# Performance work log

Hardware: AMD Instinct MI355X
Metric: run time of the kernel (lower is better)

## Reference

```python
import jax, jax.numpy as jnp
import numpy as np

B, L, C, W, NH, FS = 8, 8, 64, 32, 128, 5
PAD = FS // 2
LN_EPS = 1e-5


def _conv(x, w, b, pad):
    y = jax.lax.conv_general_dilated(x, w, (1, 1), [(pad, pad), (pad, pad)],
                                     dimension_numbers=('NCHW', 'OIHW', 'NCHW'))
    return y + b[None, :, None, None]


def _stem(x, w1, b1, lnw, lnb, w2, b2):
    # conv(fs) -> LayerNorm over [C,W,W] -> ReLU -> conv(1x1)
    y = _conv(x, w1, b1, PAD)
    mu = jnp.mean(y, axis=(1, 2, 3), keepdims=True)
    var = jnp.var(y, axis=(1, 2, 3), keepdims=True)
    y = (y - mu) * jax.lax.rsqrt(var + LN_EPS) * lnw[None] + lnb[None]
    return _conv(jax.nn.relu(y), w2, b2, 0)


def setup_inputs() -> dict:
    key = jax.random.key(0)
    ks = jax.random.split(key, 8)
    f = lambda k, shp: jax.random.normal(k, shp, jnp.float32) * 0.02
    return {
        'in_query': jax.random.normal(ks[0], (B, C, W, W), jnp.float32),
        'in_keys': jax.random.normal(ks[1], (B, L, C, W, W), jnp.float32),
        'in_values': jax.random.normal(ks[2], (B, L, C, W, W), jnp.float32),
        's_w1': f(ks[3], (C, C, FS, FS)), 's_b1': jnp.zeros((C,), jnp.float32),
        's_lnw': jnp.ones((C, W, W), jnp.float32), 's_lnb': jnp.zeros((C, W, W), jnp.float32),
        's_w2': f(ks[4], (NH, C, 1, 1)), 's_b2': jnp.zeros((NH,), jnp.float32),
        'c_w1': f(ks[5], (C, C, FS, FS)), 'c_b1': jnp.zeros((C,), jnp.float32),
        'c_lnw': jnp.ones((C, W, W), jnp.float32), 'c_lnb': jnp.zeros((C, W, W), jnp.float32),
        'c_w2': f(ks[6], (NH, C, 1, 1)), 'c_b2': jnp.zeros((NH,), jnp.float32),
    }


def reference(in_query, in_keys, in_values,
              s_w1, s_b1, s_lnw, s_lnb, s_w2, s_b2,
              c_w1, c_b1, c_lnw, c_lnb, c_w2, c_b2):
    b, c, w, h = in_query.shape
    l = in_keys.shape[1]
    # ---- spatial attention: tokens = pixels, features = channels ----
    qf = in_query.reshape(b, c, w * h).transpose(0, 2, 1)            # [B, WH, C]
    kf = in_keys.transpose(0, 1, 3, 4, 2).reshape(b, l * w * h, c)   # [B, LWH, C]
    vf = in_values.transpose(0, 1, 3, 4, 2).reshape(b, l * w * h, c)
    a_sp = jax.nn.softmax(jnp.einsum('bnc,bmc->bnm', qf, kf), axis=-1)  # [B, WH, LWH]
    sp = jnp.einsum('bnm,bmc->bnc', a_sp, vf).reshape(b, w, h, c).transpose(0, 3, 1, 2)
    # ---- channel attention: tokens = channels, features = pixels ----
    qc = in_query.reshape(b, c, w * h)                               # [B, C, WH]
    kc = in_keys.reshape(b, l * c, h * w)                            # [B, LC, WH]
    vc = in_values.reshape(b, l * c, h * w)
    a_ch = jax.nn.softmax(jnp.einsum('bcn,bmn->bcm', qc, kc), axis=-1)  # [B, C, LC]
    ch = jnp.einsum('bcm,bmn->bcn', a_ch, vc).reshape(b, c, w, h)
    # ---- conv-LN-ReLU-conv stems on residual-added branches ----
    s_attn = _stem(sp + in_query, s_w1, s_b1, s_lnw, s_lnb, s_w2, s_b2)
    c_attn = _stem(ch + in_query, c_w1, c_b1, c_lnw, c_lnb, c_w2, c_b2)
    return (s_attn, c_attn)
```

## Files before the change

### kernel.cpp

```cpp
#include <hip/hip_runtime.h>


#define LOG2E 1.44269504088896340736f

typedef __attribute__((ext_vector_type(8))) short short8;
typedef __attribute__((ext_vector_type(4))) float f4;

#define MFMA16(a, b, c) __builtin_amdgcn_mfma_f32_16x16x32_bf16(a, b, c, 0, 0, 0)

#define GLOAD_LDS16(gp, lp) __builtin_amdgcn_global_load_lds( \
    (const __attribute__((address_space(1))) void*)(gp), \
    (__attribute__((address_space(3))) void*)(lp), 16, 0, 0)

__device__ __forceinline__ unsigned short f2bf(float f) {
  union { float f; unsigned u; } v; v.f = f;
  unsigned r = v.u + 0x7FFFu + ((v.u >> 16) & 1u);
  return (unsigned short)(r >> 16);
}
__device__ __forceinline__ unsigned short f2bf_rz(float f) {
  union { float f; unsigned u; } v; v.f = f;
  return (unsigned short)(v.u >> 16);
}
__device__ __forceinline__ float bf2f(unsigned short h) {
  union { unsigned u; float f; } v; v.u = ((unsigned)h) << 16;
  return v.f;
}
__device__ __forceinline__ float exp2fast(float x) {
#if __has_builtin(__builtin_amdgcn_exp2f)
  return __builtin_amdgcn_exp2f(x);
#else
  return exp2f(x);
#endif
}

#define O_STATS 0ul
#define O_W1T   256ul
#define O_W2B   409856ul
#define O_LNW   442624ul
#define O_LNB   704768ul
#define O_QT    966912ul
#define O_KSP   2015488ul
#define O_VT    10404096ul
#define O_NUM   18792704ul
#define O_DEN   35569920ul
#define O_SP    36094208ul
#define O_PCH   40288512ul
#define O_XS    40812800ul
#define O_XC    41861376ul
#define O_YT    42909952ul

__global__ __launch_bounds__(256) void k1_prep(
    const float* __restrict__ q, const float* __restrict__ keys,
    const float* __restrict__ values,
    const float* __restrict__ sw1, const float* __restrict__ slnw,
    const float* __restrict__ slnb, const float* __restrict__ sw2,
    const float* __restrict__ cw1, const float* __restrict__ clnw,
    const float* __restrict__ clnb, const float* __restrict__ cw2,
    char* __restrict__ ws)
{
  __shared__ float T[64][65];
  const int job = blockIdx.x, t = threadIdx.x;

  if (job < 2240) {
    int kind, mat = 0, sel = 0;
    if (job < 1024)      { kind = 0; mat = job >> 4; }
    else if (job < 2048) { kind = 1; mat = (job - 1024) >> 4; }
    else if (job < 2176) { kind = 2; mat = (job - 2048) >> 4; }
    else                 { kind = 3; sel = (job - 2176) >> 4; }
    const int pt = job & 15, p0 = pt * 64;
    const float* src =
        kind == 0 ? keys : kind == 1 ? values : kind == 2 ? q
        : (sel == 0 ? slnw : sel == 1 ? slnb : sel == 2 ? clnw : clnb);
    src += (size_t)mat * 65536;

    const int r0 = t >> 4, c4 = (t & 15) * 4;
    if (kind == 1) {
      unsigned short* VTp = (unsigned short*)(ws + O_VT);
      const int b = mat >> 3, l = mat & 7;
#pragma unroll
      for (int pass = 0; pass < 4; ++pass) {
        const int r = pass * 16 + r0;
        float4 v = *(const float4*)(src + (size_t)r * 1024 + p0 + c4);
        ushort4 o;
        o.x = f2bf(v.x); o.y = f2bf(v.y); o.z = f2bf(v.z); o.w = f2bf(v.w);
        *(ushort4*)(VTp + ((size_t)b * 64 + r) * 8192 + l * 1024 + p0 + c4) = o;
      }
      return;
    }
#pragma unroll
    for (int pass = 0; pass < 4; ++pass) {
      const int r = pass * 16 + r0;
      float4 v = *(const float4*)(src + (size_t)r * 1024 + p0 + c4);
      T[r][c4] = v.x; T[r][c4 + 1] = v.y; T[r][c4 + 2] = v.z; T[r][c4 + 3] = v.w;
    }
    __syncthreads();
#pragma unroll
    for (int pass = 0; pass < 2; ++pass) {
      const int p = pass * 32 + (t >> 3), cs = (t & 7) * 8;
      short8 o;
      if (kind == 0) {
#pragma unroll
        for (int j = 0; j < 8; ++j) o[j] = (short)f2bf(T[cs + j][p] * LOG2E);
        const int b = mat >> 3, l = mat & 7;
        *(short8*)((unsigned short*)(ws + O_KSP) +
                   ((size_t)b * 8192 + l * 1024 + p0 + p) * 64 + cs) = o;
      } else if (kind == 2) {
#pragma unroll
        for (int j = 0; j < 8; ++j) o[j] = (short)f2bf(T[cs + j][p]);
        *(short8*)((unsigned short*)(ws + O_QT) +
                   ((size_t)mat * 1024 + p0 + p) * 64 + cs) = o;
      } else {
#pragma unroll
        for (int j = 0; j < 8; ++j) o[j] = (short)f2bf(T[cs + j][p]);
        unsigned long off = (sel & 1) ? O_LNB : O_LNW;
        *(short8*)((unsigned short*)(ws + off) +
                   ((size_t)(sel >> 1) * 1024 + p0 + p) * 64 + cs) = o;
      }
    }
    return;
  }

  {
    unsigned i = (job - 2240) * 256u + t;
    if (i < 204800u) {
      unsigned ci = i & 63u, co = (i >> 6) & 63u, tt = i >> 12;
      unsigned off = tt % 25u, st = tt / 25u;
      const float* w = st ? cw1 : sw1;
      ((unsigned short*)(ws + O_W1T))[i] = f2bf(w[(co * 64u + ci) * 25u + off]);
      return;
    }
    i -= 204800u;
    if (i < 16384u) {
      unsigned c = i & 63u, nh = (i >> 6) & 127u, st = i >> 13;
      const float* w = st ? cw2 : sw2;
      ((unsigned short*)(ws + O_W2B))[i] = f2bf(w[nh * 64u + c]);
    }
  }
}

__global__ __launch_bounds__(256) void k2_spat_chanS(
    const float* __restrict__ q, const float* __restrict__ keys,
    char* __restrict__ ws)
{
  __shared__ __align__(16) unsigned char SM[65536];

  if (blockIdx.x < 512) {
    unsigned short (*Kt)[4096] = (unsigned short(*)[4096])(SM);
    unsigned short (*Vt)[4096] = (unsigned short(*)[4096])(SM + 16384);
    unsigned short (*Pl)[4096] = (unsigned short(*)[4096])(SM + 32768);

    const unsigned short* QT = (const unsigned short*)(ws + O_QT);
    const unsigned short* KSP = (const unsigned short*)(ws + O_KSP);
    const unsigned short* VTg = (const unsigned short*)(ws + O_VT);
    unsigned short* NUM = (unsigned short*)(ws + O_NUM);
    float* DEN = (float*)(ws + O_DEN);

    const int b = blockIdx.x >> 6;
    const int qt = (blockIdx.x >> 4) & 3;
    const int s = blockIdx.x & 15;
    const int t = threadIdx.x;
    const int w = t >> 6, lane = t & 63;
    const int low4 = lane & 15, quad = lane >> 4;

    const unsigned short* KSPb = KSP + (size_t)b * 8192 * 64;
    const unsigned short* VTb = VTg + (size_t)b * 64 * 8192;
    const int qbase = qt * 256 + w * 64;
    const int kvbase = s * 512;

    int cn[2], cks[2], cqd[2], cl4[2];
#pragma unroll
    for (int pass = 0; pass < 2; ++pass) {
      const int c = pass * 256 + t;
      cn[pass] = c >> 7; cks[pass] = (c >> 6) & 1;
      cqd[pass] = (c >> 4) & 3; cl4[pass] = c & 15;
    }

    short8 qa[4][2];
#pragma unroll
    for (int mi = 0; mi < 4; ++mi)
#pragma unroll
      for (int ks = 0; ks < 2; ++ks)
        qa[mi][ks] = *(const short8*)(QT +
            ((size_t)(b * 1024 + qbase + mi * 16 + low4)) * 64 + ks * 32 + quad * 8);

    short8 vones;
#pragma unroll
    for (int j = 0; j < 8; ++j) vones[j] = (short)0x3F80;

    f4 accO[4][4], accD[4];
#pragma unroll
    for (int m = 0; m < 4; ++m) {
      accD[m] = (f4){0.f, 0.f, 0.f, 0.f};
#pragma unroll
      for (int n = 0; n < 4; ++n) accO[m][n] = (f4){0.f, 0.f, 0.f, 0.f};
    }

#pragma unroll
    for (int pass = 0; pass < 2; ++pass) {
      GLOAD_LDS16(KSPb + ((size_t)(kvbase + cn[pass] * 16 + cl4[pass])) * 64 +
                      cks[pass] * 32 + cqd[pass] * 8,
                  &Kt[0][(pass * 256 + w * 64) * 8]);
      GLOAD_LDS16(VTb + ((size_t)(cn[pass] * 16 + cl4[pass])) * 8192 + kvbase +
                      cks[pass] * 32 + cqd[pass] * 8,
                  &Vt[0][(pass * 256 + w * 64) * 8]);
    }

    const int pswz = ((low4 >> 2) & 3) << 1;
    for (int it = 0; it < 8; ++it) {
      const int d = it & 1;
      __syncthreads();
      if (it < 7) {
        const int kv1 = kvbase + (it + 1) * 64;
#pragma unroll
        for (int pass = 0; pass < 2; ++pass) {
          GLOAD_LDS16(KSPb + ((size_t)(kv1 + cn[pass] * 16 + cl4[pass])) * 64 +
                          cks[pass] * 32 + cqd[pass] * 8,
                      &Kt[d ^ 1][(pass * 256 + w * 64) * 8]);
          GLOAD_LDS16(VTb + ((size_t)(cn[pass] * 16 + cl4[pass])) * 8192 + kv1 +
                          cks[pass] * 32 + cqd[pass] * 8,
                      &Vt[d ^ 1][(pass * 256 + w * 64) * 8]);
        }
      }
#pragma unroll
      for (int n = 0; n < 4; ++n) {
        f4 sS[4];
#pragma unroll
        for (int mi = 0; mi < 4; ++mi) sS[mi] = (f4){0.f, 0.f, 0.f, 0.f};
#pragma unroll
        for (int ks = 0; ks < 2; ++ks) {
          short8 kb = *(const short8*)&Kt[d][((n * 2 + ks) * 64 + lane) * 8];
#pragma unroll
          for (int mi = 0; mi < 4; ++mi) sS[mi] = MFMA16(qa[mi][ks], kb, sS[mi]);
        }
        const int cpr = (((n * 2 + (low4 >> 3)) ^ (quad << 1)) << 3) + (low4 & 7);
#pragma unroll
        for (int mi = 0; mi < 4; ++mi) {
          unsigned short* pw = &Pl[w][(mi * 16 + quad * 4) * 64 + cpr];
#pragma unroll
          for (int r = 0; r < 4; ++r)
            pw[r * 64] = f2bf_rz(exp2fast(sS[mi][r]));
        }
      }
#pragma unroll
      for (int ks = 0; ks < 2; ++ks) {
        short8 vb[4];
#pragma unroll
        for (int n2 = 0; n2 < 4; ++n2)
          vb[n2] = *(const short8*)&Vt[d][((n2 * 2 + ks) * 64 + lane) * 8];
        const int cr = (((ks * 4 + quad) ^ pswz) << 3);
#pragma unroll
        for (int m = 0; m < 4; ++m) {
          short8 pa = *(const short8*)&Pl[w][(m * 16 + low4) * 64 + cr];
          accD[m] = MFMA16(pa, vones, accD[m]);
#pragma unroll
          for (int n2 = 0; n2 < 4; ++n2) accO[m][n2] = MFMA16(pa, vb[n2], accO[m][n2]);
        }
      }
    }

#pragma unroll
    for (int m = 0; m < 4; ++m)
#pragma unroll
      for (int r = 0; r < 4; ++r) {
        const int row = qbase + m * 16 + quad * 4 + r;
        const size_t base = ((size_t)(b * 1024 + row) * 16 + s);
#pragma unroll
        for (int n2 = 0; n2 < 4; ++n2)
          NUM[base * 64 + n2 * 16 + low4] = f2bf(accO[m][n2][r]);
        if (low4 == 0) DEN[base] = accD[m][r];
      }
    return;
  }

  {
    float* Sp = (float*)(ws + O_SP);
    const int bid = blockIdx.x - 512;
    const int b = bid >> 4, colT = (bid >> 2) & 3, kt = bid & 3;
    const int t = threadIdx.x, w = t >> 6, lane = t & 63;
    const int low4 = lane & 15, quad = lane >> 4;
    const int dl = lane >> 1, dh = lane & 1;
    const int k00 = kt * 256;

    f4 acc[4][2];
#pragma unroll
    for (int m = 0; m < 4; ++m)
#pragma unroll
      for (int n = 0; n < 2; ++n) acc[m][n] = (f4){0.f, 0.f, 0.f, 0.f};

    auto stageAll = [&](int bo, int k0) {
#pragma unroll
      for (int gi = 0; gi < 4; ++gi) {
        const int g = w + gi * 4;
        const int n = g >> 1, sub = g & 1;
        const int l = sub * 32 + dl;
        const float* gp = keys + (size_t)(b * 512 + colT * 128 + n * 16 + (l & 15)) * 1024
                          + k0 + (l >> 4) * 8 + dh * 4;
        GLOAD_LDS16(gp, SM + bo + (size_t)(n * 128 + sub * 64) * 16);
      }
#pragma unroll
      for (int gi = 0; gi < 2; ++gi) {
        const int g = w + gi * 4;
        const int m = g >> 1, sub = g & 1;
        const int l = sub * 32 + dl;
        const float* gp = q + (size_t)(b * 64 + m * 16 + (l & 15)) * 1024
                          + k0 + (l >> 4) * 8 + dh * 4;
        GLOAD_LDS16(gp, SM + bo + 16384 + (size_t)(m * 128 + sub * 64) * 16);
      }
    };

    stageAll(0, k00);
    for (int it = 0; it < 8; ++it) {
      const int bo = (it & 1) * 24576;
      const char* cb = (const char*)SM + bo;
      __syncthreads();
      if (it < 7) stageAll(bo ^ 24576, k00 + (it + 1) * 32);

      short8 ah[4], al[4];
#pragma unroll
      for (int m = 0; m < 4; ++m) {
        const float* fp = (const float*)(cb + 16384 + (size_t)(m * 128 + lane * 2) * 16);
        float4 u0 = ((const float4*)fp)[0];
        float4 u1 = ((const float4*)fp)[1];
        float vv[8] = {u0.x, u0.y, u0.z, u0.w, u1.x, u1.y, u1.z, u1.w};
#pragma unroll
        for (int j = 0; j < 8; ++j) {
          float sv = vv[j] * LOG2E;
          unsigned short hi = f2bf(sv);
          ah[m][j] = (short)hi;
          al[m][j] = (short)f2bf(sv - bf2f(hi));
        }
      }
#pragma unroll
      for (int n2 = 0; n2 < 2; ++n2) {
        const int n = w * 2 + n2;
        const float* fp = (const float*)(cb + (size_t)(n * 128 + lane * 2) * 16);
        float4 u0 = ((const float4*)fp)[0];
        float4 u1 = ((const float4*)fp)[1];
        float vv[8] = {u0.x, u0.y, u0.z, u0.w, u1.x, u1.y, u1.z, u1.w};
        short8 bh, bl;
#pragma unroll
        for (int j = 0; j < 8; ++j) {
          unsigned short hi = f2bf(vv[j]);
          bh[j] = (short)hi;
          bl[j] = (short)f2bf(vv[j] - bf2f(hi));
        }
#pragma unroll
        for (int m = 0; m < 4; ++m) {
          acc[m][n2] = MFMA16(ah[m], bh, acc[m][n2]);
          acc[m][n2] = MFMA16(al[m], bh, acc[m][n2]);
          acc[m][n2] = MFMA16(ah[m], bl, acc[m][n2]);
        }
      }
    }

#pragma unroll
    for (int m = 0; m < 4; ++m)
#pragma unroll
      for (int n2 = 0; n2 < 2; ++n2)
#pragma unroll
        for (int r = 0; r < 4; ++r) {
          const int row = m * 16 + quad * 4 + r;
          const int col = colT * 128 + (w * 2 + n2) * 16 + low4;
          Sp[(((size_t)kt * 8 + b) * 64 + row) * 512 + col] = acc[m][n2][r];
        }
  }
}

__global__ __launch_bounds__(256) void k3_fin_soft(char* __restrict__ ws)
{
  if (blockIdx.x < 512) {
    const unsigned short* NUM = (const unsigned short*)(ws + O_NUM);
    const float* DEN = (const float*)(ws + O_DEN);
    const unsigned short* QT = (const unsigned short*)(ws + O_QT);
    unsigned short* Xs = (unsigned short*)(ws + O_XS);

    const unsigned i = blockIdx.x * 256u + threadIdx.x;
    const int c0 = (i & 15) * 4;
    const unsigned row = i >> 4;

    float dtot = 0.f;
#pragma unroll
    for (int sq = 0; sq < 4; ++sq) {
      float4 dv = *(const float4*)(DEN + (size_t)row * 16 + sq * 4);
      dtot += dv.x + dv.y + dv.z + dv.w;
    }
    float n4[4] = {0.f, 0.f, 0.f, 0.f};
#pragma unroll
    for (int s = 0; s < 16; ++s) {
      ushort4 pv = *(const ushort4*)(NUM + ((size_t)row * 16 + s) * 64 + c0);
      n4[0] += bf2f(pv.x); n4[1] += bf2f(pv.y);
      n4[2] += bf2f(pv.z); n4[3] += bf2f(pv.w);
    }
    const float rd = 1.0f / dtot;
    size_t ob = (size_t)row * 64 + c0;
    ushort4 qv = *(const ushort4*)(QT + ob);
    ushort4 o4;
    o4.x = f2bf(n4[0] * rd + bf2f(qv.x));
    o4.y = f2bf(n4[1] * rd + bf2f(qv.y));
    o4.z = f2bf(n4[2] * rd + bf2f(qv.z));
    o4.w = f2bf(n4[3] * rd + bf2f(qv.w));
    *(ushort4*)(Xs + ob) = o4;
    return;
  }

  {
    const float* Sp = (const float*)(ws + O_SP);
    unsigned short* P = (unsigned short*)(ws + O_PCH);
    const int bid = blockIdx.x - 512;
    const int b = bid >> 2, rt = bid & 3;
    const int row = rt * 16 + (threadIdx.x >> 4), tc = threadIdx.x & 15;

    float sv[32];
    float mx = -1e30f;
#pragma unroll
    for (int jj = 0; jj < 32; ++jj) {
      const int col = jj * 16 + tc;
      size_t base = ((size_t)b * 64 + row) * 512 + col;
      float v = Sp[base] + Sp[base + 262144] + Sp[base + 524288] + Sp[base + 786432];
      sv[jj] = v;
      mx = fmaxf(mx, v);
    }
#pragma unroll
    for (int o = 1; o < 16; o <<= 1) mx = fmaxf(mx, __shfl_xor(mx, o, 64));
    float sum = 0.f;
#pragma unroll
    for (int jj = 0; jj < 32; ++jj) {
      float e = exp2fast(sv[jj] - mx);
      sv[jj] = e;
      sum += e;
    }
#pragma unroll
    for (int o = 1; o < 16; o <<= 1) sum += __shfl_xor(sum, o, 64);
    const float rs = 1.0f / sum;
#pragma unroll
    for (int jj = 0; jj < 32; ++jj)
      P[((size_t)b * 64 + row) * 512 + jj * 16 + tc] = f2bf(sv[jj] * rs);
  }
}

__device__ __forceinline__ void conv5_body(char* ws, const float* b1p, int s, int bid)
{
  __shared__ float Hbuf[2][16][65];
  __shared__ float red[2][2];

  const int b = bid >> 5, pt = bid & 31;
  const int w = threadIdx.x >> 6, lane = threadIdx.x & 63;
  const int low4 = lane & 15, quad = lane >> 4;
  const int wsub = w & 1, half = w >> 1;

  const unsigned short* X = (const unsigned short*)(ws + (s ? O_XC : O_XS));
  const unsigned short* W1t = (const unsigned short*)(ws + O_W1T);
  unsigned short* Yt = (unsigned short*)(ws + O_YT);
  float* stats = (float*)(ws + O_STATS);

  const int p = pt * 32 + wsub * 16 + low4;
  const int y0 = p >> 5, x0 = p & 31;

  f4 acc[4];
#pragma unroll
  for (int m = 0; m < 4; ++m) acc[m] = (f4){0.f, 0.f, 0.f, 0.f};

  const int o0 = half ? 13 : 0, o1 = half ? 25 : 13;
  for (int off = o0; off < o1; ++off) {
    const int dy = off / 5 - 2, dx = off % 5 - 2;
    const int ys = y0 + dy, xs = x0 + dx;
    const bool valid = ((unsigned)ys < 32u) & ((unsigned)xs < 32u);
    const int psrc = valid ? (p + dy * 32 + dx) : p;
    const unsigned short* xp = X + ((size_t)(b * 1024 + psrc)) * 64;
    const unsigned short* wp = W1t + ((size_t)((s * 25 + off) * 64)) * 64;
#pragma unroll
    for (int ks = 0; ks < 2; ++ks) {
      short8 bv = *(const short8*)(xp + ks * 32 + quad * 8);
      if (!valid) bv = (short8)0;
#pragma unroll
      for (int m = 0; m < 4; ++m) {
        short8 av = *(const short8*)(wp + (m * 16 + low4) * 64 + ks * 32 + quad * 8);
        acc[m] = MFMA16(av, bv, acc[m]);
      }
    }
  }

  if (half) {
#pragma unroll
    for (int m = 0; m < 4; ++m)
#pragma unroll
      for (int r = 0; r < 4; ++r)
        Hbuf[wsub][low4][m * 16 + quad * 4 + r] = acc[m][r];
  }
  __syncthreads();
  if (!half) {
    float ls = 0.f, ls2 = 0.f;
#pragma unroll
    for (int m = 0; m < 4; ++m)
#pragma unroll
      for (int r = 0; r < 4; ++r) {
        const int co = m * 16 + quad * 4 + r;
        float y = acc[m][r] + Hbuf[wsub][low4][co] + b1p[co];
        Yt[((size_t)((s * 8 + b) * 1024 + p)) * 64 + co] = f2bf(y);
        ls += y; ls2 += y * y;
      }
#pragma unroll
    for (int o = 1; o < 64; o <<= 1) {
      ls += __shfl_xor(ls, o, 64);
      ls2 += __shfl_xor(ls2, o, 64);
    }
    if (lane == 0) { red[0][wsub] = ls; red[1][wsub] = ls2; }
  }
  __syncthreads();
  if (threadIdx.x == 0) {
    atomicAdd(&stats[(s * 8 + b) * 2 + 0], red[0][0] + red[0][1]);
    atomicAdd(&stats[(s * 8 + b) * 2 + 1], red[1][0] + red[1][1]);
  }
}

__device__ __forceinline__ void final_body(char* ws, const float* b2p,
                                           float* out, int s, int bid)
{
  const int b = bid >> 5, pt = bid & 31;
  const int w = threadIdx.x >> 6, lane = threadIdx.x & 63;
  const int low4 = lane & 15, quad = lane >> 4;
  const int p2 = pt * 32 + (w & 1) * 16 + low4;
  const int nh0 = (w >> 1) * 64;

  const unsigned short* Yt = (const unsigned short*)(ws + O_YT);
  const unsigned short* LNW = (const unsigned short*)(ws + O_LNW);
  const unsigned short* LNB = (const unsigned short*)(ws + O_LNB);
  const unsigned short* W2b = (const unsigned short*)(ws + O_W2B);
  const float* stats = (const float*)(ws + O_STATS);

  const float inv = 1.0f / 65536.0f;
  const float mu = stats[(s * 8 + b) * 2 + 0] * inv;
  const float ms = stats[(s * 8 + b) * 2 + 1] * inv;
  const float rsig = rsqrtf(ms - mu * mu + 1e-5f);

  f4 acc[4];
#pragma unroll
  for (int m = 0; m < 4; ++m) acc[m] = (f4){0.f, 0.f, 0.f, 0.f};

#pragma unroll
  for (int ks = 0; ks < 2; ++ks) {
    size_t yo = ((size_t)((s * 8 + b) * 1024 + p2)) * 64 + ks * 32 + quad * 8;
    size_t lo = ((size_t)(s * 1024 + p2)) * 64 + ks * 32 + quad * 8;
    short8 yv = *(const short8*)(Yt + yo);
    short8 lw8 = *(const short8*)(LNW + lo);
    short8 lb8 = *(const short8*)(LNB + lo);
    short8 zv;
#pragma unroll
    for (int j = 0; j < 8; ++j) {
      float z = (bf2f((unsigned short)yv[j]) - mu) * rsig * bf2f((unsigned short)lw8[j]) +
                bf2f((unsigned short)lb8[j]);
      zv[j] = (short)f2bf(fmaxf(z, 0.f));
    }
#pragma unroll
    for (int m = 0; m < 4; ++m) {
      short8 a = *(const short8*)(W2b + ((size_t)(s * 128 + nh0 + m * 16 + low4)) * 64 + ks * 32 + quad * 8);
      acc[m] = MFMA16(a, zv, acc[m]);
    }
  }
#pragma unroll
  for (int m = 0; m < 4; ++m)
#pragma unroll
    for (int r = 0; r < 4; ++r) {
      const int nh = nh0 + m * 16 + quad * 4 + r;
      out[((size_t)((s * 8 + b) * 128 + nh)) * 1024 + p2] = acc[m][r] + b2p[nh];
    }
}

__global__ __launch_bounds__(256) void k4_conv5s_chanB(
    const float* __restrict__ values, char* __restrict__ ws,
    const float* __restrict__ sb1)
{
  if (blockIdx.x < 256) { conv5_body(ws, sb1, 0, blockIdx.x); return; }

  const unsigned short* P = (const unsigned short*)(ws + O_PCH);
  const unsigned short* QT = (const unsigned short*)(ws + O_QT);
  unsigned short* Xc = (unsigned short*)(ws + O_XC);

  const int bid = blockIdx.x - 256;
  const int b = bid >> 4, pt = bid & 15;
  const int w = threadIdx.x >> 6, lane = threadIdx.x & 63;
  const int low4 = lane & 15, quad = lane >> 4;
  const int p = pt * 64 + w * 16 + low4;

  f4 acc[4];
#pragma unroll
  for (int m = 0; m < 4; ++m) acc[m] = (f4){0.f, 0.f, 0.f, 0.f};

  const float* vbase = values + (size_t)b * 524288 + p;
  for (int ks = 0; ks < 16; ++ks) {
    short8 vbv;
    const float* vp = vbase + (size_t)(ks * 32 + quad * 8) * 1024;
#pragma unroll
    for (int j = 0; j < 8; ++j) vbv[j] = (short)f2bf(vp[(size_t)j * 1024]);
#pragma unroll
    for (int m = 0; m < 4; ++m) {
      short8 a = *(const short8*)(P + ((size_t)(b * 64 + m * 16 + low4)) * 512 + ks * 32 + quad * 8);
      acc[m] = MFMA16(a, vbv, acc[m]);
    }
  }
#pragma unroll
  for (int m = 0; m < 4; ++m)
#pragma unroll
    for (int r = 0; r < 4; ++r) {
      const int c = m * 16 + quad * 4 + r;
      size_t o = ((size_t)(b * 1024 + p)) * 64 + c;
      Xc[o] = f2bf(acc[m][r] + bf2f(QT[o]));
    }
}

__global__ __launch_bounds__(256) void k5_conv5c_finS(
    char* __restrict__ ws, const float* __restrict__ cb1,
    const float* __restrict__ sb2, float* __restrict__ out)
{
  if (blockIdx.x < 256) { conv5_body(ws, cb1, 1, blockIdx.x); return; }
  final_body(ws, sb2, out, 0, blockIdx.x - 256);
}

__global__ __launch_bounds__(256) void k6_finC(
    char* __restrict__ ws, const float* __restrict__ cb2,
    float* __restrict__ out)
{
  final_body(ws, cb2, out, 1, blockIdx.x);
}

extern "C" void kernel_launch(void* const* d_in, const int* in_sizes, int n_in,
                              void* d_out, int out_size, void* d_ws, size_t ws_size,
                              hipStream_t stream)
{
  const float* q    = (const float*)d_in[0];
  const float* keys = (const float*)d_in[1];
  const float* vals = (const float*)d_in[2];
  const float* sw1  = (const float*)d_in[3];
  const float* sb1  = (const float*)d_in[4];
  const float* slnw = (const float*)d_in[5];
  const float* slnb = (const float*)d_in[6];
  const float* sw2  = (const float*)d_in[7];
  const float* sb2  = (const float*)d_in[8];
  const float* cw1  = (const float*)d_in[9];
  const float* cb1  = (const float*)d_in[10];
  const float* clnw = (const float*)d_in[11];
  const float* clnb = (const float*)d_in[12];
  const float* cw2  = (const float*)d_in[13];
  const float* cb2  = (const float*)d_in[14];
  char* ws = (char*)d_ws;

  (void)hipMemsetAsync(ws + O_STATS, 0, 256, stream);
  k1_prep<<<3104, 256, 0, stream>>>(q, keys, vals, sw1, slnw, slnb, sw2,
                                    cw1, clnw, clnb, cw2, ws);
  k2_spat_chanS<<<640, 256, 0, stream>>>(q, keys, ws);
  k3_fin_soft<<<544, 256, 0, stream>>>(ws);
  k4_conv5s_chanB<<<384, 256, 0, stream>>>(vals, ws, sb1);
  k5_conv5c_finS<<<512, 256, 0, stream>>>(ws, cb1, sb2, (float*)d_out);
  k6_finC<<<256, 256, 0, stream>>>(ws, cb2, (float*)d_out);
}
```

Baseline: 211.4 us.

## Fuse channel softmax into channel-attention PV and regroup stage kernels

The channel-attention softmax is now computed inside the kernel that multiplies by the values. The unnormalized bf16 probabilities stay in LDS and the 1/sum normalization is applied at output, so the global P buffer round-trip goes away. The spatial-attention QK MFMA swaps its operands so each lane writes four packed bf16 probabilities with one 8-byte store into a padded LDS tile, replacing the XOR swizzle. The conv and final stages are regrouped into two kernels, cutting the launch count from six to five. In exchange, the channel blocks recompute the softmax per pixel tile (16x redundant Sp reads) and use about 67 KB of LDS, which may reduce occupancy.

```diff
diff --git a/kernel.cpp b/kernel.cpp
--- a/kernel.cpp
+++ b/kernel.cpp
@@ -17,13 +17,16 @@
   unsigned r = v.u + 0x7FFFu + ((v.u >> 16) & 1u);
   return (unsigned short)(r >> 16);
 }
-__device__ __forceinline__ unsigned short f2bf_rz(float f) {
-  union { float f; unsigned u; } v; v.f = f;
-  return (unsigned short)(v.u >> 16);
-}
 __device__ __forceinline__ float bf2f(unsigned short h) {
   union { unsigned u; float f; } v; v.u = ((unsigned)h) << 16;
   return v.f;
+}
+__device__ __forceinline__ unsigned pack2_rz(float a, float b) {
+  union { float f; unsigned u; } x, y; x.f = a; y.f = b;
+  return (x.u >> 16) | (y.u & 0xFFFF0000u);
+}
+__device__ __forceinline__ unsigned pack2_rne(float a, float b) {
+  return (unsigned)f2bf(a) | ((unsigned)f2bf(b) << 16);
 }
 __device__ __forceinline__ float exp2fast(float x) {
 #if __has_builtin(__builtin_amdgcn_exp2f)
@@ -44,7 +47,6 @@
 #define O_NUM   18792704ul
 #define O_DEN   35569920ul
 #define O_SP    36094208ul
-#define O_PCH   40288512ul
 #define O_XS    40812800ul
 #define O_XC    41861376ul
 #define O_YT    42909952ul
@@ -142,12 +144,11 @@
     const float* __restrict__ q, const float* __restrict__ keys,
     char* __restrict__ ws)
 {
-  __shared__ __align__(16) unsigned char SM[65536];
+  __shared__ __align__(16) unsigned char SM[67584];
 
   if (blockIdx.x < 512) {
-    unsigned short (*Kt)[4096] = (unsigned short(*)[4096])(SM);
-    unsigned short (*Vt)[4096] = (unsigned short(*)[4096])(SM + 16384);
-    unsigned short (*Pl)[4096] = (unsigned short(*)[4096])(SM + 32768);
+    unsigned short* KtB = (unsigned short*)SM;
+    unsigned short* VtB = (unsigned short*)(SM + 16384);
 
     const unsigned short* QT = (const unsigned short*)(ws + O_QT);
     const unsigned short* KSP = (const unsigned short*)(ws + O_KSP);
@@ -162,6 +163,8 @@
     const int w = t >> 6, lane = t & 63;
     const int low4 = lane & 15, quad = lane >> 4;
 
+    unsigned short* Pw = (unsigned short*)(SM + 32768) + w * 4352;
+
     const unsigned short* KSPb = KSP + (size_t)b * 8192 * 64;
     const unsigned short* VTb = VTg + (size_t)b * 64 * 8192;
     const int qbase = qt * 256 + w * 64;
@@ -199,26 +202,26 @@
     for (int pass = 0; pass < 2; ++pass) {
       GLOAD_LDS16(KSPb + ((size_t)(kvbase + cn[pass] * 16 + cl4[pass])) * 64 +
                       cks[pass] * 32 + cqd[pass] * 8,
-                  &Kt[0][(pass * 256 + w * 64) * 8]);
+                  &KtB[(pass * 256 + w * 64) * 8]);
       GLOAD_LDS16(VTb + ((size_t)(cn[pass] * 16 + cl4[pass])) * 8192 + kvbase +
                       cks[pass] * 32 + cqd[pass] * 8,
-                  &Vt[0][(pass * 256 + w * 64) * 8]);
-    }
-
-    const int pswz = ((low4 >> 2) & 3) << 1;
+                  &VtB[(pass * 256 + w * 64) * 8]);
+    }
+
     for (int it = 0; it < 8; ++it) {
       const int d = it & 1;
       __syncthreads();
       if (it < 7) {
         const int kv1 = kvbase + (it + 1) * 64;
+        const int dn = (d ^ 1) * 4096;
 #pragma unroll
         for (int pass = 0; pass < 2; ++pass) {
           GLOAD_LDS16(KSPb + ((size_t)(kv1 + cn[pass] * 16 + cl4[pass])) * 64 +
                           cks[pass] * 32 + cqd[pass] * 8,
-                      &Kt[d ^ 1][(pass * 256 + w * 64) * 8]);
+                      &KtB[dn + (pass * 256 + w * 64) * 8]);
           GLOAD_LDS16(VTb + ((size_t)(cn[pass] * 16 + cl4[pass])) * 8192 + kv1 +
                           cks[pass] * 32 + cqd[pass] * 8,
-                      &Vt[d ^ 1][(pass * 256 + w * 64) * 8]);
+                      &VtB[dn + (pass * 256 + w * 64) * 8]);
         }
       }
 #pragma unroll
@@ -228,17 +231,20 @@
         for (int mi = 0; mi < 4; ++mi) sS[mi] = (f4){0.f, 0.f, 0.f, 0.f};
 #pragma unroll
         for (int ks = 0; ks < 2; ++ks) {
-          short8 kb = *(const short8*)&Kt[d][((n * 2 + ks) * 64 + lane) * 8];
-#pragma unroll
-          for (int mi = 0; mi < 4; ++mi) sS[mi] = MFMA16(qa[mi][ks], kb, sS[mi]);
-        }
-        const int cpr = (((n * 2 + (low4 >> 3)) ^ (quad << 1)) << 3) + (low4 & 7);
+          short8 kb = *(const short8*)&KtB[d * 4096 + ((n * 2 + ks) * 64 + lane) * 8];
+#pragma unroll
+          for (int mi = 0; mi < 4; ++mi) sS[mi] = MFMA16(kb, qa[mi][ks], sS[mi]);
+        }
 #pragma unroll
         for (int mi = 0; mi < 4; ++mi) {
-          unsigned short* pw = &Pl[w][(mi * 16 + quad * 4) * 64 + cpr];
-#pragma unroll
-          for (int r = 0; r < 4; ++r)
-            pw[r * 64] = f2bf_rz(exp2fast(sS[mi][r]));
+          float e0 = exp2fast(sS[mi][0]);
+          float e1 = exp2fast(sS[mi][1]);
+          float e2 = exp2fast(sS[mi][2]);
+          float e3 = exp2fast(sS[mi][3]);
+          uint2 pk;
+          pk.x = pack2_rz(e0, e1);
+          pk.y = pack2_rz(e2, e3);
+          *(uint2*)&Pw[(mi * 16 + low4) * 68 + n * 16 + quad * 4] = pk;
         }
       }
 #pragma unroll
@@ -246,11 +252,10 @@
         short8 vb[4];
 #pragma unroll
         for (int n2 = 0; n2 < 4; ++n2)
-          vb[n2] = *(const short8*)&Vt[d][((n2 * 2 + ks) * 64 + lane) * 8];
-        const int cr = (((ks * 4 + quad) ^ pswz) << 3);
+          vb[n2] = *(const short8*)&VtB[d * 4096 + ((n2 * 2 + ks) * 64 + lane) * 8];
 #pragma unroll
         for (int m = 0; m < 4; ++m) {
-          short8 pa = *(const short8*)&Pl[w][(m * 16 + low4) * 64 + cr];
+          short8 pa = *(const short8*)&Pw[(m * 16 + low4) * 68 + ks * 32 + quad * 8];
           accD[m] = MFMA16(pa, vones, accD[m]);
 #pragma unroll
           for (int n2 = 0; n2 < 4; ++n2) accO[m][n2] = MFMA16(pa, vb[n2], accO[m][n2]);
@@ -366,12 +371,16 @@
   }
 }
 
-__global__ __launch_bounds__(256) void k3_fin_soft(char* __restrict__ ws)
-{
+__global__ __launch_bounds__(256) void k3_finS_chanB(
+    const float* __restrict__ values, char* __restrict__ ws)
+{
+  __shared__ __align__(16) unsigned short Pl[64 * 524];
+  __shared__ float RS[64];
+  const unsigned short* QT = (const unsigned short*)(ws + O_QT);
+
   if (blockIdx.x < 512) {
     const unsigned short* NUM = (const unsigned short*)(ws + O_NUM);
     const float* DEN = (const float*)(ws + O_DEN);
-    const unsigned short* QT = (const unsigned short*)(ws + O_QT);
     unsigned short* Xs = (unsigned short*)(ws + O_XS);
 
     const unsigned i = blockIdx.x * 256u + threadIdx.x;
@@ -405,36 +414,81 @@
 
   {
     const float* Sp = (const float*)(ws + O_SP);
-    unsigned short* P = (unsigned short*)(ws + O_PCH);
+    unsigned short* Xc = (unsigned short*)(ws + O_XC);
+
     const int bid = blockIdx.x - 512;
-    const int b = bid >> 2, rt = bid & 3;
-    const int row = rt * 16 + (threadIdx.x >> 4), tc = threadIdx.x & 15;
-
-    float sv[32];
+    const int b = bid >> 4, pt = bid & 15;
+    const int t = threadIdx.x;
+
+    const int row = t >> 2, sub = t & 3;
+    const float* sp0 = Sp + ((size_t)b * 64 + row) * 512;
     float mx = -1e30f;
 #pragma unroll
-    for (int jj = 0; jj < 32; ++jj) {
-      const int col = jj * 16 + tc;
-      size_t base = ((size_t)b * 64 + row) * 512 + col;
-      float v = Sp[base] + Sp[base + 262144] + Sp[base + 524288] + Sp[base + 786432];
-      sv[jj] = v;
-      mx = fmaxf(mx, v);
-    }
-#pragma unroll
-    for (int o = 1; o < 16; o <<= 1) mx = fmaxf(mx, __shfl_xor(mx, o, 64));
+    for (int i = 0; i < 32; ++i) {
+      const int col = i * 16 + sub * 4;
+      float4 v0 = *(const float4*)(sp0 + col);
+      float4 v1 = *(const float4*)(sp0 + 262144 + col);
+      float4 v2 = *(const float4*)(sp0 + 524288 + col);
+      float4 v3 = *(const float4*)(sp0 + 786432 + col);
+      float s0 = v0.x + v1.x + v2.x + v3.x;
+      float s1 = v0.y + v1.y + v2.y + v3.y;
+      float s2 = v0.z + v1.z + v2.z + v3.z;
+      float s3 = v0.w + v1.w + v2.w + v3.w;
+      mx = fmaxf(mx, fmaxf(fmaxf(s0, s1), fmaxf(s2, s3)));
+    }
+    mx = fmaxf(mx, __shfl_xor(mx, 1, 64));
+    mx = fmaxf(mx, __shfl_xor(mx, 2, 64));
     float sum = 0.f;
 #pragma unroll
-    for (int jj = 0; jj < 32; ++jj) {
-      float e = exp2fast(sv[jj] - mx);
-      sv[jj] = e;
-      sum += e;
-    }
-#pragma unroll
-    for (int o = 1; o < 16; o <<= 1) sum += __shfl_xor(sum, o, 64);
-    const float rs = 1.0f / sum;
-#pragma unroll
-    for (int jj = 0; jj < 32; ++jj)
-      P[((size_t)b * 64 + row) * 512 + jj * 16 + tc] = f2bf(sv[jj] * rs);
+    for (int i = 0; i < 32; ++i) {
+      const int col = i * 16 + sub * 4;
+      float4 v0 = *(const float4*)(sp0 + col);
+      float4 v1 = *(const float4*)(sp0 + 262144 + col);
+      float4 v2 = *(const float4*)(sp0 + 524288 + col);
+      float4 v3 = *(const float4*)(sp0 + 786432 + col);
+      float e0 = exp2fast(v0.x + v1.x + v2.x + v3.x - mx);
+      float e1 = exp2fast(v0.y + v1.y + v2.y + v3.y - mx);
+      float e2 = exp2fast(v0.z + v1.z + v2.z + v3.z - mx);
+      float e3 = exp2fast(v0.w + v1.w + v2.w + v3.w - mx);
+      sum += (e0 + e1) + (e2 + e3);
+      uint2 pk;
+      pk.x = pack2_rne(e0, e1);
+      pk.y = pack2_rne(e2, e3);
+      *(uint2*)&Pl[row * 524 + col] = pk;
+    }
+    sum += __shfl_xor(sum, 1, 64);
+    sum += __shfl_xor(sum, 2, 64);
+    if (sub == 0) RS[row] = 1.0f / sum;
+    __syncthreads();
+
+    const int w = t >> 6, lane = t & 63;
+    const int low4 = lane & 15, quad = lane >> 4;
+    const int p = pt * 64 + w * 16 + low4;
+
+    f4 acc[4];
+#pragma unroll
+    for (int m = 0; m < 4; ++m) acc[m] = (f4){0.f, 0.f, 0.f, 0.f};
+
+    const float* vbase = values + (size_t)b * 524288 + p;
+    for (int ks = 0; ks < 16; ++ks) {
+      short8 vbv;
+      const float* vp = vbase + (size_t)(ks * 32 + quad * 8) * 1024;
+#pragma unroll
+      for (int j = 0; j < 8; ++j) vbv[j] = (short)f2bf(vp[(size_t)j * 1024]);
+#pragma unroll
+      for (int m = 0; m < 4; ++m) {
+        short8 a = *(const short8*)&Pl[(m * 16 + low4) * 524 + ks * 32 + quad * 8];
+        acc[m] = MFMA16(a, vbv, acc[m]);
+      }
+    }
+#pragma unroll
+    for (int m = 0; m < 4; ++m)
+#pragma unroll
+      for (int r = 0; r < 4; ++r) {
+        const int c = m * 16 + quad * 4 + r;
+        size_t o = ((size_t)(b * 1024 + p)) * 64 + c;
+        Xc[o] = f2bf(acc[m][r] * RS[c] + bf2f(QT[o]));
+      }
   }
 }
 
@@ -566,61 +620,21 @@
     }
 }
 
-__global__ __launch_bounds__(256) void k4_conv5s_chanB(
-    const float* __restrict__ values, char* __restrict__ ws,
-    const float* __restrict__ sb1)
-{
-  if (blockIdx.x < 256) { conv5_body(ws, sb1, 0, blockIdx.x); return; }
-
-  const unsigned short* P = (const unsigned short*)(ws + O_PCH);
-  const unsigned short* QT = (const unsigned short*)(ws + O_QT);
-  unsigned short* Xc = (unsigned short*)(ws + O_XC);
-
-  const int bid = blockIdx.x - 256;
-  const int b = bid >> 4, pt = bid & 15;
-  const int w = threadIdx.x >> 6, lane = threadIdx.x & 63;
-  const int low4 = lane & 15, quad = lane >> 4;
-  const int p = pt * 64 + w * 16 + low4;
-
-  f4 acc[4];
-#pragma unroll
-  for (int m = 0; m < 4; ++m) acc[m] = (f4){0.f, 0.f, 0.f, 0.f};
-
-  const float* vbase = values + (size_t)b * 524288 + p;
-  for (int ks = 0; ks < 16; ++ks) {
-    short8 vbv;
-    const float* vp = vbase + (size_t)(ks * 32 + quad * 8) * 1024;
-#pragma unroll
-    for (int j = 0; j < 8; ++j) vbv[j] = (short)f2bf(vp[(size_t)j * 1024]);
-#pragma unroll
-    for (int m = 0; m < 4; ++m) {
-      short8 a = *(const short8*)(P + ((size_t)(b * 64 + m * 16 + low4)) * 512 + ks * 32 + quad * 8);
-      acc[m] = MFMA16(a, vbv, acc[m]);
-    }
-  }
-#pragma unroll
-  for (int m = 0; m < 4; ++m)
-#pragma unroll
-    for (int r = 0; r < 4; ++r) {
-      const int c = m * 16 + quad * 4 + r;
-      size_t o = ((size_t)(b * 1024 + p)) * 64 + c;
-      Xc[o] = f2bf(acc[m][r] + bf2f(QT[o]));
-    }
-}
-
-__global__ __launch_bounds__(256) void k5_conv5c_finS(
-    char* __restrict__ ws, const float* __restrict__ cb1,
-    const float* __restrict__ sb2, float* __restrict__ out)
-{
-  if (blockIdx.x < 256) { conv5_body(ws, cb1, 1, blockIdx.x); return; }
-  final_body(ws, sb2, out, 0, blockIdx.x - 256);
-}
-
-__global__ __launch_bounds__(256) void k6_finC(
-    char* __restrict__ ws, const float* __restrict__ cb2,
-    float* __restrict__ out)
-{
-  final_body(ws, cb2, out, 1, blockIdx.x);
+__global__ __launch_bounds__(256) void k4_conv(char* __restrict__ ws,
+                                               const float* __restrict__ sb1,
+                                               const float* __restrict__ cb1)
+{
+  const int s = blockIdx.x >> 8;
+  conv5_body(ws, s ? cb1 : sb1, s, blockIdx.x & 255);
+}
+
+__global__ __launch_bounds__(256) void k5_final(char* __restrict__ ws,
+                                                const float* __restrict__ sb2,
+                                                const float* __restrict__ cb2,
+                                                float* __restrict__ out)
+{
+  const int s = blockIdx.x >> 8;
+  final_body(ws, s ? cb2 : sb2, out, s, blockIdx.x & 255);
 }
 
 extern "C" void kernel_launch(void* const* d_in, const int* in_sizes, int n_in,
@@ -648,8 +662,7 @@
   k1_prep<<<3104, 256, 0, stream>>>(q, keys, vals, sw1, slnw, slnb, sw2,
                                     cw1, clnw, clnb, cw2, ws);
   k2_spat_chanS<<<640, 256, 0, stream>>>(q, keys, ws);
-  k3_fin_soft<<<544, 256, 0, stream>>>(ws);
-  k4_conv5s_chanB<<<384, 256, 0, stream>>>(vals, ws, sb1);
-  k5_conv5c_finS<<<512, 256, 0, stream>>>(ws, cb1, sb2, (float*)d_out);
-  k6_finC<<<256, 256, 0, stream>>>(ws, cb2, (float*)d_out);
-}
+  k3_finS_chanB<<<640, 256, 0, stream>>>(vals, ws);
+  k4_conv<<<512, 256, 0, stream>>>(ws, sb1, cb1);
+  k5_final<<<512, 256, 0, stream>>>(ws, sb2, cb2, (float*)d_out);
+}
```

Result: slower. 279.0 us (+32.0%).
